# Kernel optimization log

Hardware: AMD Instinct MI355X
Metric: run time of the kernel (lower is better)

The kernel has to match this reference:

```python
import jax, jax.numpy as jnp
import numpy as np

N, M, D, DV = 8192, 8192, 128, 128
N_MASK = 1_000_000


def setup_inputs() -> dict:
    key = jax.random.key(0)
    kq, kk, kv, kr, kc = jax.random.split(key, 5)
    query = jax.random.normal(kq, (N, D), dtype=jnp.float32)
    k = jax.random.normal(kk, (M, D), dtype=jnp.float32)
    value = jax.random.normal(kv, (M, DV), dtype=jnp.float32)
    mask_rows = jax.random.randint(kr, (N_MASK,), 0, N, dtype=jnp.int64 if jax.config.jax_enable_x64 else jnp.int32)
    mask_cols = jax.random.randint(kc, (N_MASK,), 0, M, dtype=jnp.int64 if jax.config.jax_enable_x64 else jnp.int32)
    return {"query": query, "key": k, "value": value,
            "mask_rows": mask_rows, "mask_cols": mask_cols}


def reference(query, key, value, mask_rows, mask_cols):
    d = query.shape[1]
    # [N, M] score matrix: q @ k^T / sqrt(d)
    scores = (query @ key.T) / jnp.sqrt(jnp.asarray(d, dtype=query.dtype))
    # scatter -inf at masked coordinates (torch: scaled[mask[0], mask[1]] = -inf)
    scores = scores.at[mask_rows, mask_cols].set(-jnp.inf)
    attn = jax.nn.softmax(scores, axis=1)
    return attn @ value
```

## Files before the change

kernel.cpp:

```cpp
#include <hip/hip_runtime.h>
#include <stdint.h>

#define NQ 8192
#define NM 8192
#define DD 128
#define DVD 128
#define BK 64
#define NKB64 (NM / BK)
#define BQ 128
#define NQB (NQ / BQ)

typedef float f32x4 __attribute__((ext_vector_type(4)));
typedef short s16x8 __attribute__((ext_vector_type(8)));
typedef __fp16 fp16x2 __attribute__((ext_vector_type(2)));
union FragU { uint32_t u[4]; s16x8 v; };
union H2U { fp16x2 h; uint32_t u; };

__device__ __forceinline__ uint32_t bf16rne(float x) {
  uint32_t u = __float_as_uint(x);
  return (u + 0x7FFFu + ((u >> 16) & 1u)) >> 16;
}
__device__ __forceinline__ uint32_t pk_bf16_rhu(float a, float b) {
  return ((__float_as_uint(a) + 0x8000u) >> 16) |
         ((__float_as_uint(b) + 0x8000u) & 0xFFFF0000u);
}

__device__ __forceinline__ void glds16(const void* g, void* l) {
  __builtin_amdgcn_global_load_lds((const __attribute__((address_space(1))) uint32_t*)g,
                                   (__attribute__((address_space(3))) uint32_t*)l, 16, 0, 0);
}

#define SZ_MASK ((size_t)(NM / 64) * NQ * 8)
#define OFF_K   (SZ_MASK)
#define SZ_KB   ((size_t)NM * DD * 2)
#define OFF_V   (OFF_K + SZ_KB)
#define OFF_OP  (OFF_V + SZ_KB)
#define SZ_OPH  ((size_t)NQ * DVD * 2)
#define SZ_L1   ((size_t)NQ * 4)

__global__ void mask_scatter_kernel(const int* __restrict__ mr, const int* __restrict__ mc,
                                    int n, unsigned int* __restrict__ maskT) {
  int i = blockIdx.x * 256 + threadIdx.x;
  if (i < n) {
    int r = mr[i], c = mc[i];
    size_t w = ((size_t)(c >> 6) * NQ + r) * 2 + ((c >> 5) & 1);
    atomicOr(&maskT[w], 1u << (c & 31));
  }
}

__global__ __launch_bounds__(256) void conv_kernel(const float* __restrict__ K,
                                                   const float* __restrict__ V,
                                                   uint8_t* __restrict__ Kswz,
                                                   uint8_t* __restrict__ Vtswz,
                                                   uint4* __restrict__ maskT4) {
  __shared__ float Vf[64][132];
  int b = blockIdx.x;
  int tid = threadIdx.x;
  if (b < 512) {
    int t = b * 256 + tid;
    int key = t >> 4, c = t & 15;
    const float* s = K + (size_t)key * DD + 8 * c;
    float4 a = *(const float4*)s, bb = *(const float4*)(s + 4);
    uint4 d;
    d.x = bf16rne(a.x) | (bf16rne(a.y) << 16);
    d.y = bf16rne(a.z) | (bf16rne(a.w) << 16);
    d.z = bf16rne(bb.x) | (bf16rne(bb.y) << 16);
    d.w = bf16rne(bb.z) | (bf16rne(bb.w) << 16);
    size_t off = (size_t)(key >> 6) * 16384 + (size_t)(key & 63) * 256 +
                 (size_t)((c ^ (key & 15)) << 4);
    *(uint4*)(Kswz + off) = d;
  } else if (b < 640) {
    int kb = b - 512;
#pragma unroll
    for (int i = 0; i < 8; ++i) {
      int idx = tid + 256 * i;
      int key = idx >> 5, c4 = idx & 31;
      float4 f = *(const float4*)(V + ((size_t)kb * 64 + key) * DVD + 4 * c4);
      *(float4*)&Vf[key][4 * c4] = f;
    }
    __syncthreads();
#pragma unroll
    for (int j = 0; j < 4; ++j) {
      int s = tid + 256 * j;
      int dv = s >> 3, c = s & 7;
      uint4 d;
      uint32_t* dw = (uint32_t*)&d;
#pragma unroll
      for (int w = 0; w < 4; ++w) {
        int k0 = 8 * c + 2 * w;
        dw[w] = bf16rne(Vf[k0][dv]) | (bf16rne(Vf[k0 + 1][dv]) << 16);
      }
      size_t off = (size_t)kb * 16384 + (size_t)dv * 128 + (size_t)((c ^ (dv & 7)) << 4);
      *(uint4*)(Vtswz + off) = d;
    }
  } else {
    size_t i = (size_t)(b - 640) * 256 + tid;
    uint4 z = {0, 0, 0, 0};
    maskT4[i] = z;
    maskT4[i + 131072] = z;
    maskT4[i + 262144] = z;
    maskT4[i + 393216] = z;
  }
}

__global__ __launch_bounds__(256, 2) void attn_kernel(
    const float* __restrict__ Q, const uint8_t* __restrict__ Kswz,
    const uint8_t* __restrict__ Vtswz, const unsigned int* __restrict__ maskT,
    __fp16* __restrict__ Opart, float* __restrict__ lsum, int lg) {
  const int bid = blockIdx.x;
  const int span = bid & ((1 << lg) - 1);
  const int qblk = bid >> lg;
  const int niter = NKB64 >> lg;
  const int kb0 = span * niter;

  const int tid = threadIdx.x;
  const int wid = tid >> 6, lane = tid & 63;
  const int g = lane >> 4, qi = lane & 15;
  const int qw = qblk * BQ + wid * 32;

  __shared__ uint8_t Klds[16384];
  __shared__ uint8_t Vlds[16384];
  __shared__ uint32_t Psc[8][16][36];

  const float SC = 0.08838834764831845f * 1.4426950408889634f;

  s16x8 qfrag[2][4];
#pragma unroll
  for (int qt = 0; qt < 2; ++qt)
#pragma unroll
    for (int ks = 0; ks < 4; ++ks) {
      const float* qs = Q + (size_t)(qw + 16 * qt + qi) * DD + 32 * ks + 8 * g;
      float4 a = *(const float4*)qs, b = *(const float4*)(qs + 4);
      FragU fu;
      fu.u[0] = bf16rne(a.x * SC) | (bf16rne(a.y * SC) << 16);
      fu.u[1] = bf16rne(a.z * SC) | (bf16rne(a.w * SC) << 16);
      fu.u[2] = bf16rne(b.x * SC) | (bf16rne(b.y * SC) << 16);
      fu.u[3] = bf16rne(b.z * SC) | (bf16rne(b.w * SC) << 16);
      qfrag[qt][ks] = fu.v;
    }

  f32x4 accO[8][2];
#pragma unroll
  for (int dt = 0; dt < 8; ++dt)
#pragma unroll
    for (int qt = 0; qt < 2; ++qt) accO[dt][qt] = (f32x4)0.f;
  f32x4 accL[2] = {(f32x4)0.f, (f32x4)0.f};

  FragU onesu;
  onesu.u[0] = onesu.u[1] = onesu.u[2] = onesu.u[3] = 0x3F803F80u;
  const s16x8 onesfrag = onesu.v;

  const s16x8* Kv = (const s16x8*)Klds;
  const s16x8* Vv = (const s16x8*)Vlds;

  for (int it = 0; it < niter; ++it) {
    const int kb = kb0 + it;
    __syncthreads();
    {
      const uint8_t* kt = Kswz + (size_t)kb * 16384;
      const uint8_t* vt = Vtswz + (size_t)kb * 16384;
#pragma unroll
      for (int s = 0; s < 4; ++s) {
        glds16(kt + s * 4096 + (size_t)tid * 16, Klds + s * 4096 + wid * 1024);
        glds16(vt + s * 4096 + (size_t)tid * 16, Vlds + s * 4096 + wid * 1024);
      }
    }
    uint2 wm[2];
#pragma unroll
    for (int qt = 0; qt < 2; ++qt)
      wm[qt] = *(const uint2*)&maskT[((size_t)kb * NQ + qw + 16 * qt + qi) * 2];
    __syncthreads();

    f32x4 sf[2][4];
#pragma unroll
    for (int qt = 0; qt < 2; ++qt)
#pragma unroll
      for (int kt = 0; kt < 4; ++kt) sf[qt][kt] = (f32x4)0.f;
#pragma unroll
    for (int kt = 0; kt < 4; ++kt)
#pragma unroll
      for (int ks = 0; ks < 4; ++ks) {
        s16x8 kf = Kv[(16 * kt + qi) * 16 + ((g + 4 * ks) ^ qi)];
        sf[0][kt] = __builtin_amdgcn_mfma_f32_16x16x32_bf16(kf, qfrag[0][ks], sf[0][kt], 0, 0, 0);
        sf[1][kt] = __builtin_amdgcn_mfma_f32_16x16x32_bf16(kf, qfrag[1][ks], sf[1][kt], 0, 0, 0);
      }

    if (__ballot((wm[0].x | wm[0].y | wm[1].x | wm[1].y) != 0)) {
#pragma unroll
      for (int qt = 0; qt < 2; ++qt)
#pragma unroll
        for (int kt = 0; kt < 4; ++kt)
#pragma unroll
          for (int r = 0; r < 4; ++r) {
            int kl = 16 * kt + 4 * g + r;
            unsigned int w = (kl & 32) ? wm[qt].y : wm[qt].x;
            if ((w >> (kl & 31)) & 1u) sf[qt][kt][r] = -3.0e38f;
          }
    }

    s16x8 pfrag[2][2];
#pragma unroll
    for (int qt = 0; qt < 2; ++qt) {
      uint32_t* row = &Psc[wid * 2 + qt][qi][0];
#pragma unroll
      for (int kt = 0; kt < 4; ++kt) {
        float p0 = exp2f(sf[qt][kt][0]), p1 = exp2f(sf[qt][kt][1]);
        float p2 = exp2f(sf[qt][kt][2]), p3 = exp2f(sf[qt][kt][3]);
        uint2 pk;
        pk.x = pk_bf16_rhu(p0, p1);
        pk.y = pk_bf16_rhu(p2, p3);
        *(uint2*)&row[8 * kt + 2 * g] = pk;
      }
      pfrag[qt][0] = *(const s16x8*)&row[4 * g];
      pfrag[qt][1] = *(const s16x8*)&row[16 + 4 * g];
    }

#pragma unroll
    for (int kh = 0; kh < 2; ++kh) {
      accL[0] = __builtin_amdgcn_mfma_f32_16x16x32_bf16(onesfrag, pfrag[0][kh], accL[0], 0, 0, 0);
      accL[1] = __builtin_amdgcn_mfma_f32_16x16x32_bf16(onesfrag, pfrag[1][kh], accL[1], 0, 0, 0);
    }

#pragma unroll
    for (int dt = 0; dt < 8; ++dt) {
#pragma unroll
      for (int kh = 0; kh < 2; ++kh) {
        s16x8 vf = Vv[(16 * dt + qi) * 8 + ((4 * kh + g) ^ (qi & 7))];
        accO[dt][0] = __builtin_amdgcn_mfma_f32_16x16x32_bf16(vf, pfrag[0][kh], accO[dt][0], 0, 0, 0);
        accO[dt][1] = __builtin_amdgcn_mfma_f32_16x16x32_bf16(vf, pfrag[1][kh], accO[dt][1], 0, 0, 0);
      }
    }
  }

#pragma unroll
  for (int qt = 0; qt < 2; ++qt) {
    int q = qw + 16 * qt + qi;
#pragma unroll
    for (int dt = 0; dt < 8; ++dt) {
      H2U h0, h1;
      h0.h = __builtin_amdgcn_cvt_pkrtz(accO[dt][qt][0], accO[dt][qt][1]);
      h1.h = __builtin_amdgcn_cvt_pkrtz(accO[dt][qt][2], accO[dt][qt][3]);
      uint2 st = {h0.u, h1.u};
      *(uint2*)(Opart + ((size_t)span * NQ + q) * DVD + 16 * dt + 4 * g) = st;
    }
    if (g == 0) lsum[(size_t)span * NQ + q] = accL[qt][0];
  }
}

__global__ __launch_bounds__(256) void merge_kernel(const __fp16* __restrict__ Opart,
                                                    const float* __restrict__ lsum,
                                                    float* __restrict__ out, int nsplit) {
  int idx = blockIdx.x * 256 + threadIdx.x;
  int row = idx >> 5, c4 = idx & 31;
  float den = 0.f;
  f32x4 o = (f32x4)0.f;
  for (int p = 0; p < nsplit; ++p) {
    den += lsum[(size_t)p * NQ + row];
    uint2 h = *(const uint2*)(Opart + ((size_t)p * NQ + row) * DVD + 4 * c4);
    H2U a, b;
    a.u = h.x; b.u = h.y;
    o[0] += (float)a.h[0]; o[1] += (float)a.h[1];
    o[2] += (float)b.h[0]; o[3] += (float)b.h[1];
  }
  o *= (1.f / den);
  ((f32x4*)out)[idx] = o;
}

extern "C" void kernel_launch(void* const* d_in, const int* in_sizes, int n_in,
                              void* d_out, int out_size, void* d_ws, size_t ws_size,
                              hipStream_t stream) {
  const float* Q = (const float*)d_in[0];
  const float* K = (const float*)d_in[1];
  const float* V = (const float*)d_in[2];
  const int* mr = (const int*)d_in[3];
  const int* mc = (const int*)d_in[4];
  const int nmask = in_sizes[3];

  uint8_t* ws = (uint8_t*)d_ws;
  unsigned int* maskT = (unsigned int*)ws;
  uint8_t* Kswz = ws + OFF_K;
  uint8_t* Vtswz = ws + OFF_V;
  __fp16* Opart = (__fp16*)(ws + OFF_OP);

  int lg;
  if (ws_size >= OFF_OP + 16 * (SZ_OPH + SZ_L1)) lg = 4;
  else if (ws_size >= OFF_OP + 8 * (SZ_OPH + SZ_L1)) lg = 3;
  else if (ws_size >= OFF_OP + 4 * (SZ_OPH + SZ_L1)) lg = 2;
  else if (ws_size >= OFF_OP + 2 * (SZ_OPH + SZ_L1)) lg = 1;
  else lg = 0;
  int nsplit = 1 << lg;
  float* lsum = (float*)(ws + OFF_OP + (size_t)nsplit * SZ_OPH);

  conv_kernel<<<1152, 256, 0, stream>>>(K, V, Kswz, Vtswz, (uint4*)maskT);
  mask_scatter_kernel<<<(nmask + 255) / 256, 256, 0, stream>>>(mr, mc, nmask, maskT);
  attn_kernel<<<NQB * nsplit, 256, 0, stream>>>(Q, Kswz, Vtswz, maskT, Opart, lsum, lg);
  merge_kernel<<<NQ * DVD / 4 / 256, 256, 0, stream>>>(Opart, lsum, (float*)d_out, nsplit);
}
```

Before: 181.0 us.

## Fuse mask scatter into conversion kernel, raise attention occupancy, strength-reduce addressing

The mask zeroing moves to hipMemsetAsync, and the mask scatter is folded into the K/V conversion kernel, which removes one kernel launch. The attention kernel's launch bounds go from 2 to 3 blocks per SIMD, which forces the compiler to use fewer registers and risks spills. Loop addressing is strength-reduced with precomputed pointers that are incremented each iteration. The first score MFMA now takes a zero accumulator directly instead of zero-initialising it, and the bf16 packing uses a byte permute instruction.

```diff
diff --git a/kernel.cpp b/kernel.cpp
--- a/kernel.cpp
+++ b/kernel.cpp
@@ -20,9 +20,9 @@
   uint32_t u = __float_as_uint(x);
   return (u + 0x7FFFu + ((u >> 16) & 1u)) >> 16;
 }
-__device__ __forceinline__ uint32_t pk_bf16_rhu(float a, float b) {
-  return ((__float_as_uint(a) + 0x8000u) >> 16) |
-         ((__float_as_uint(b) + 0x8000u) & 0xFFFF0000u);
+__device__ __forceinline__ uint32_t pk2(float a, float b) {
+  return __builtin_amdgcn_perm(__float_as_uint(b) + 0x8000u,
+                               __float_as_uint(a) + 0x8000u, 0x07060302u);
 }
 
 __device__ __forceinline__ void glds16(const void* g, void* l) {
@@ -38,21 +38,11 @@
 #define SZ_OPH  ((size_t)NQ * DVD * 2)
 #define SZ_L1   ((size_t)NQ * 4)
 
-__global__ void mask_scatter_kernel(const int* __restrict__ mr, const int* __restrict__ mc,
-                                    int n, unsigned int* __restrict__ maskT) {
-  int i = blockIdx.x * 256 + threadIdx.x;
-  if (i < n) {
-    int r = mr[i], c = mc[i];
-    size_t w = ((size_t)(c >> 6) * NQ + r) * 2 + ((c >> 5) & 1);
-    atomicOr(&maskT[w], 1u << (c & 31));
-  }
-}
-
-__global__ __launch_bounds__(256) void conv_kernel(const float* __restrict__ K,
-                                                   const float* __restrict__ V,
-                                                   uint8_t* __restrict__ Kswz,
-                                                   uint8_t* __restrict__ Vtswz,
-                                                   uint4* __restrict__ maskT4) {
+__global__ __launch_bounds__(256) void conv_scatter_kernel(
+    const float* __restrict__ K, const float* __restrict__ V,
+    uint8_t* __restrict__ Kswz, uint8_t* __restrict__ Vtswz,
+    const int* __restrict__ mr, const int* __restrict__ mc, int nmask,
+    unsigned int* __restrict__ maskT) {
   __shared__ float Vf[64][132];
   int b = blockIdx.x;
   int tid = threadIdx.x;
@@ -95,15 +85,15 @@
     }
   } else {
     size_t i = (size_t)(b - 640) * 256 + tid;
-    uint4 z = {0, 0, 0, 0};
-    maskT4[i] = z;
-    maskT4[i + 131072] = z;
-    maskT4[i + 262144] = z;
-    maskT4[i + 393216] = z;
-  }
-}
-
-__global__ __launch_bounds__(256, 2) void attn_kernel(
+    if (i < (size_t)nmask) {
+      int r = mr[i], c = mc[i];
+      size_t w = ((size_t)(c >> 6) * NQ + r) * 2 + ((c >> 5) & 1);
+      atomicOr(&maskT[w], 1u << (c & 31));
+    }
+  }
+}
+
+__global__ __launch_bounds__(256, 3) void attn_kernel(
     const float* __restrict__ Q, const uint8_t* __restrict__ Kswz,
     const uint8_t* __restrict__ Vtswz, const unsigned int* __restrict__ maskT,
     __fp16* __restrict__ Opart, float* __restrict__ lsum, int lg) {
@@ -145,6 +135,7 @@
 #pragma unroll
     for (int qt = 0; qt < 2; ++qt) accO[dt][qt] = (f32x4)0.f;
   f32x4 accL[2] = {(f32x4)0.f, (f32x4)0.f};
+  const f32x4 z4 = (f32x4)0.f;
 
   FragU onesu;
   onesu.u[0] = onesu.u[1] = onesu.u[2] = onesu.u[3] = 0x3F803F80u;
@@ -152,67 +143,83 @@
 
   const s16x8* Kv = (const s16x8*)Klds;
   const s16x8* Vv = (const s16x8*)Vlds;
+  const s16x8* kp[4];
+#pragma unroll
+  for (int ks = 0; ks < 4; ++ks) kp[ks] = Kv + qi * 16 + ((g + 4 * ks) ^ qi);
+  const s16x8* vp[2];
+#pragma unroll
+  for (int kh = 0; kh < 2; ++kh) vp[kh] = Vv + qi * 8 + ((4 * kh + g) ^ (qi & 7));
+  uint32_t* prow[2];
+  const s16x8* pread[2];
+#pragma unroll
+  for (int qt = 0; qt < 2; ++qt) {
+    prow[qt] = &Psc[wid * 2 + qt][qi][0];
+    pread[qt] = (const s16x8*)&prow[qt][4 * g];
+  }
+
+  const uint8_t* ktp = Kswz + (size_t)kb0 * 16384 + (size_t)tid * 16;
+  const uint8_t* vtp = Vtswz + (size_t)kb0 * 16384 + (size_t)tid * 16;
+  uint8_t* kld = Klds + wid * 1024;
+  uint8_t* vld = Vlds + wid * 1024;
+  const uint2* mp0 = (const uint2*)maskT + (size_t)kb0 * NQ + qw + qi;
+  const uint2* mp1 = mp0 + 16;
 
   for (int it = 0; it < niter; ++it) {
-    const int kb = kb0 + it;
     __syncthreads();
-    {
-      const uint8_t* kt = Kswz + (size_t)kb * 16384;
-      const uint8_t* vt = Vtswz + (size_t)kb * 16384;
-#pragma unroll
-      for (int s = 0; s < 4; ++s) {
-        glds16(kt + s * 4096 + (size_t)tid * 16, Klds + s * 4096 + wid * 1024);
-        glds16(vt + s * 4096 + (size_t)tid * 16, Vlds + s * 4096 + wid * 1024);
-      }
-    }
-    uint2 wm[2];
-#pragma unroll
-    for (int qt = 0; qt < 2; ++qt)
-      wm[qt] = *(const uint2*)&maskT[((size_t)kb * NQ + qw + 16 * qt + qi) * 2];
+#pragma unroll
+    for (int s = 0; s < 4; ++s) {
+      glds16(ktp + s * 4096, kld + s * 4096);
+      glds16(vtp + s * 4096, vld + s * 4096);
+    }
+    uint2 wm0 = *mp0, wm1 = *mp1;
+    ktp += 16384; vtp += 16384; mp0 += NQ; mp1 += NQ;
     __syncthreads();
 
     f32x4 sf[2][4];
 #pragma unroll
-    for (int qt = 0; qt < 2; ++qt)
-#pragma unroll
-      for (int kt = 0; kt < 4; ++kt) sf[qt][kt] = (f32x4)0.f;
-#pragma unroll
-    for (int kt = 0; kt < 4; ++kt)
-#pragma unroll
-      for (int ks = 0; ks < 4; ++ks) {
-        s16x8 kf = Kv[(16 * kt + qi) * 16 + ((g + 4 * ks) ^ qi)];
+    for (int kt = 0; kt < 4; ++kt) {
+      {
+        s16x8 kf = kp[0][kt * 256];
+        sf[0][kt] = __builtin_amdgcn_mfma_f32_16x16x32_bf16(kf, qfrag[0][0], z4, 0, 0, 0);
+        sf[1][kt] = __builtin_amdgcn_mfma_f32_16x16x32_bf16(kf, qfrag[1][0], z4, 0, 0, 0);
+      }
+#pragma unroll
+      for (int ks = 1; ks < 4; ++ks) {
+        s16x8 kf = kp[ks][kt * 256];
         sf[0][kt] = __builtin_amdgcn_mfma_f32_16x16x32_bf16(kf, qfrag[0][ks], sf[0][kt], 0, 0, 0);
         sf[1][kt] = __builtin_amdgcn_mfma_f32_16x16x32_bf16(kf, qfrag[1][ks], sf[1][kt], 0, 0, 0);
       }
-
-    if (__ballot((wm[0].x | wm[0].y | wm[1].x | wm[1].y) != 0)) {
-#pragma unroll
-      for (int qt = 0; qt < 2; ++qt)
+    }
+
+    if (__ballot((wm0.x | wm0.y | wm1.x | wm1.y) != 0)) {
+#pragma unroll
+      for (int qt = 0; qt < 2; ++qt) {
+        uint2 wm = qt ? wm1 : wm0;
 #pragma unroll
         for (int kt = 0; kt < 4; ++kt)
 #pragma unroll
           for (int r = 0; r < 4; ++r) {
             int kl = 16 * kt + 4 * g + r;
-            unsigned int w = (kl & 32) ? wm[qt].y : wm[qt].x;
+            unsigned int w = (kl & 32) ? wm.y : wm.x;
             if ((w >> (kl & 31)) & 1u) sf[qt][kt][r] = -3.0e38f;
           }
+      }
     }
 
     s16x8 pfrag[2][2];
 #pragma unroll
     for (int qt = 0; qt < 2; ++qt) {
-      uint32_t* row = &Psc[wid * 2 + qt][qi][0];
 #pragma unroll
       for (int kt = 0; kt < 4; ++kt) {
         float p0 = exp2f(sf[qt][kt][0]), p1 = exp2f(sf[qt][kt][1]);
         float p2 = exp2f(sf[qt][kt][2]), p3 = exp2f(sf[qt][kt][3]);
         uint2 pk;
-        pk.x = pk_bf16_rhu(p0, p1);
-        pk.y = pk_bf16_rhu(p2, p3);
-        *(uint2*)&row[8 * kt + 2 * g] = pk;
-      }
-      pfrag[qt][0] = *(const s16x8*)&row[4 * g];
-      pfrag[qt][1] = *(const s16x8*)&row[16 + 4 * g];
+        pk.x = pk2(p0, p1);
+        pk.y = pk2(p2, p3);
+        *(uint2*)&prow[qt][8 * kt + 2 * g] = pk;
+      }
+      pfrag[qt][0] = pread[qt][0];
+      pfrag[qt][1] = pread[qt][4];
     }
 
 #pragma unroll
@@ -225,7 +232,7 @@
     for (int dt = 0; dt < 8; ++dt) {
 #pragma unroll
       for (int kh = 0; kh < 2; ++kh) {
-        s16x8 vf = Vv[(16 * dt + qi) * 8 + ((4 * kh + g) ^ (qi & 7))];
+        s16x8 vf = vp[kh][dt * 128];
         accO[dt][0] = __builtin_amdgcn_mfma_f32_16x16x32_bf16(vf, pfrag[0][kh], accO[dt][0], 0, 0, 0);
         accO[dt][1] = __builtin_amdgcn_mfma_f32_16x16x32_bf16(vf, pfrag[1][kh], accO[dt][1], 0, 0, 0);
       }
@@ -291,8 +298,9 @@
   int nsplit = 1 << lg;
   float* lsum = (float*)(ws + OFF_OP + (size_t)nsplit * SZ_OPH);
 
-  conv_kernel<<<1152, 256, 0, stream>>>(K, V, Kswz, Vtswz, (uint4*)maskT);
-  mask_scatter_kernel<<<(nmask + 255) / 256, 256, 0, stream>>>(mr, mc, nmask, maskT);
+  hipMemsetAsync(maskT, 0, SZ_MASK, stream);
+  conv_scatter_kernel<<<640 + (nmask + 255) / 256, 256, 0, stream>>>(
+      K, V, Kswz, Vtswz, mr, mc, nmask, maskT);
   attn_kernel<<<NQB * nsplit, 256, 0, stream>>>(Q, Kswz, Vtswz, maskT, Opart, lsum, lg);
   merge_kernel<<<NQ * DVD / 4 / 256, 256, 0, stream>>>(Opart, lsum, (float*)d_out, nsplit);
 }
```

Result: no change. 183.1 us (+1.2%).
